# Optimization experiments

Measured on AMD Instinct MI355X. Metric: run time of the kernel, lower is better.

The kernel has to match this reference:

```python
import math
import jax, jax.numpy as jnp
import numpy as np

B, S, D, H = 4, 2048, 1024, 16
DK = D // H


def setup_inputs() -> dict:
    key = jax.random.key(0)
    ks = jax.random.split(key, 12)
    scale = 1.0 / math.sqrt(D)
    inp = {
        "query": jax.random.normal(ks[0], (B, S, D), jnp.float32),
        "key": jax.random.normal(ks[1], (B, S, D), jnp.float32),
        "value": jax.random.normal(ks[2], (B, S, D), jnp.float32),
        # causal mask, broadcasts over batch and (after unsqueeze) heads
        "mask": jnp.tril(jnp.ones((1, S, S), jnp.int32)),
        # torch Linear weights: [out_features, in_features]
        "Wq": jax.random.uniform(ks[3], (D, D), jnp.float32, -scale, scale),
        "bq": jax.random.uniform(ks[4], (D,), jnp.float32, -scale, scale),
        "Wk": jax.random.uniform(ks[5], (D, D), jnp.float32, -scale, scale),
        "bk": jax.random.uniform(ks[6], (D,), jnp.float32, -scale, scale),
        "Wv": jax.random.uniform(ks[7], (D, D), jnp.float32, -scale, scale),
        "bv": jax.random.uniform(ks[8], (D,), jnp.float32, -scale, scale),
        "Wo": jax.random.uniform(ks[9], (D, D), jnp.float32, -scale, scale),
        "bo": jax.random.uniform(ks[10], (D,), jnp.float32, -scale, scale),
    }
    return inp


def _proj(x, W, b):
    # torch Linear: x @ W.T + b, then split heads -> [B, H, S, DK]
    y = jnp.einsum('bsd,ed->bse', x, W) + b
    return y.reshape(x.shape[0], x.shape[1], H, DK).transpose(0, 2, 1, 3)


def reference(query, key, value, mask, Wq, bq, Wk, bk, Wv, bv, Wo, bo):
    q = _proj(query, Wq, bq)
    k = _proj(key, Wk, bk)
    v = _proj(value, Wv, bv)
    # scores: [B, H, S, S]
    scores = jnp.einsum('bhqd,bhkd->bhqk', q, k) / math.sqrt(DK)
    m = mask[:, None, :, :]  # mask.unsqueeze(1) -> broadcast over heads
    scores = jnp.where(m == 0, jnp.float32(-1e9), scores)
    prob = jax.nn.softmax(scores, axis=-1)
    # dropout is identity in eval mode
    x = jnp.einsum('bhqk,bhkd->bhqd', prob, v)
    x = x.transpose(0, 2, 1, 3).reshape(query.shape[0], -1, H * DK)
    return jnp.einsum('bsd,ed->bse', x, Wo) + bo
```

## Files before the change

kernel.cpp:

```cpp
#include <hip/hip_runtime.h>
#include <hip/hip_bf16.h>

#define DI __device__ __forceinline__

typedef __bf16 bf16x8 __attribute__((ext_vector_type(8)));
typedef unsigned short u16x8 __attribute__((ext_vector_type(8)));
typedef unsigned short u16x4 __attribute__((ext_vector_type(4)));
typedef unsigned int u32x4 __attribute__((ext_vector_type(4)));
typedef float f32x4 __attribute__((ext_vector_type(4)));
typedef float f32x16 __attribute__((ext_vector_type(16)));

constexpr int kB = 4, kS = 2048, kD = 1024, kH = 16;
constexpr int kM = kB * kS;

DI unsigned short f2bf(float f) {
  union { float f; unsigned u; } x; x.f = f;
  unsigned r = x.u + 0x7fffu + ((x.u >> 16) & 1u);
  return (unsigned short)(r >> 16);
}

DI f32x4 mfma16(u16x8 a, u16x8 b, f32x4 c) {
  return __builtin_amdgcn_mfma_f32_16x16x32_bf16(
      __builtin_bit_cast(bf16x8, a), __builtin_bit_cast(bf16x8, b), c, 0, 0, 0);
}
DI f32x16 mfma32(u16x8 a, u16x8 b, f32x16 c) {
  return __builtin_amdgcn_mfma_f32_32x32x16_bf16(
      __builtin_bit_cast(bf16x8, a), __builtin_bit_cast(bf16x8, b), c, 0, 0, 0);
}

DI void gload16(const unsigned short* g, unsigned short* l) {
  __builtin_amdgcn_global_load_lds(
      (__attribute__((address_space(1))) void*)g,
      (__attribute__((address_space(3))) void*)l, 16, 0, 0);
}

DI unsigned pkbf(float lo, float hi) {
  unsigned r;
  asm("v_cvt_pk_bf16_f32 %0, %1, %2" : "=v"(r) : "v"(lo), "v"(hi));
  return r;
}

__global__ __launch_bounds__(256) void conv_w(const float* __restrict__ s0,
                                              const float* __restrict__ s1,
                                              const float* __restrict__ s2,
                                              const float* __restrict__ s3,
                                              unsigned short* __restrict__ d) {
  const int j = blockIdx.y;
  const float* s = j == 0 ? s0 : j == 1 ? s1 : j == 2 ? s2 : s3;
  const size_t i = ((size_t)blockIdx.x * 256 + threadIdx.x) * 8;
  f32x4 a = *reinterpret_cast<const f32x4*>(s + i);
  f32x4 b = *reinterpret_cast<const f32x4*>(s + i + 4);
  u16x8 o;
#pragma unroll
  for (int jj = 0; jj < 4; ++jj) { o[jj] = f2bf(a[jj]); o[jj + 4] = f2bf(b[jj]); }
  *reinterpret_cast<u16x8*>(d + (size_t)j * 1048576 + i) = o;
}

__global__ __launch_bounds__(256) void proj_gemm(
    const float* __restrict__ A, const unsigned short* __restrict__ W,
    const float* __restrict__ bias, float scale, int vmode,
    unsigned short* __restrict__ O) {
  constexpr int K = kD, N = kD;
  __shared__ unsigned short As[128][64];
  __shared__ unsigned short Bs[2][128][64];

  const int lin = blockIdx.y * 8 + blockIdx.x;
  const int rm = (lin & 7) * 64 + (lin >> 3);
  const int n0 = (rm & 7) * 128, m0 = (rm >> 3) * 128;

  const int t = threadIdx.x;
  const int wave = t >> 6, lane = t & 63;
  const int wr = (wave >> 1) * 64, wc = (wave & 1) * 64;
  const int lrow = lane & 15, lkq = lane >> 4;

  const int rl = lane >> 3;
  const int bcs8 = ((lane & 7) ^ rl) * 8;
  const unsigned short* bsrc = W + ((size_t)(n0 + wave * 32 + rl)) * K + bcs8;
  unsigned short* bl = &Bs[0][0][0] + wave * 2048;

  const int ar_r = t >> 3, ar_c = t & 7;
  const int asw = (ar_c ^ (ar_r & 7)) * 8;
  const float* abase = A + (size_t)(m0 + ar_r) * K + ar_c * 8;

  f32x4 ar0[4], ar1[4];
#pragma unroll
  for (int i = 0; i < 4; ++i) {
    const float* ap = abase + (size_t)i * 32 * K;
    ar0[i] = *reinterpret_cast<const f32x4*>(ap);
    ar1[i] = *reinterpret_cast<const f32x4*>(ap + 4);
  }
#pragma unroll
  for (int i = 0; i < 4; ++i) gload16(bsrc + (size_t)i * 8 * K, bl + i * 512);

  f32x4 acc[4][4];
#pragma unroll
  for (int m = 0; m < 4; ++m)
#pragma unroll
    for (int n = 0; n < 4; ++n) acc[m][n] = f32x4{0.f, 0.f, 0.f, 0.f};

  for (int kt = 0; kt < K; kt += 64) {
    const int cb = (kt >> 6) & 1;
    __syncthreads();
#pragma unroll
    for (int i = 0; i < 4; ++i) {
      u32x4 w;
      w[0] = pkbf(ar0[i][0], ar0[i][1]);
      w[1] = pkbf(ar0[i][2], ar0[i][3]);
      w[2] = pkbf(ar1[i][0], ar1[i][1]);
      w[3] = pkbf(ar1[i][2], ar1[i][3]);
      *reinterpret_cast<u32x4*>(&As[ar_r + i * 32][asw]) = w;
    }
    __syncthreads();

    if (kt + 64 < K) {
#pragma unroll
      for (int i = 0; i < 4; ++i)
        gload16(bsrc + (size_t)i * 8 * K + kt + 64, bl + (cb ^ 1) * 8192 + i * 512);
#pragma unroll
      for (int i = 0; i < 4; ++i) {
        const float* ap = abase + (size_t)i * 32 * K + kt + 64;
        ar0[i] = *reinterpret_cast<const f32x4*>(ap);
        ar1[i] = *reinterpret_cast<const f32x4*>(ap + 4);
      }
    }

    u16x8 af[4][2], bf[4][2];
#pragma unroll
    for (int m = 0; m < 4; ++m) {
      const int row = wr + m * 16 + lrow;
#pragma unroll
      for (int kk = 0; kk < 2; ++kk)
        af[m][kk] = *reinterpret_cast<const u16x8*>(
            &As[row][((kk * 4 + lkq) ^ (row & 7)) * 8]);
    }
#pragma unroll
    for (int n = 0; n < 4; ++n) {
      const int row = wc + n * 16 + lrow;
#pragma unroll
      for (int kk = 0; kk < 2; ++kk)
        bf[n][kk] = *reinterpret_cast<const u16x8*>(
            &Bs[cb][row][((kk * 4 + lkq) ^ (row & 7)) * 8]);
    }
#pragma unroll
    for (int kk = 0; kk < 2; ++kk)
#pragma unroll
      for (int m = 0; m < 4; ++m)
#pragma unroll
        for (int n = 0; n < 4; ++n)
          acc[m][n] = mfma16(af[m][kk], bf[n][kk], acc[m][n]);
  }

#pragma unroll
  for (int n = 0; n < 4; ++n) {
    const int gc = n0 + wc + n * 16 + lrow;
    const float bvv = bias[gc];
#pragma unroll
    for (int m = 0; m < 4; ++m) {
      const int gr = m0 + wr + m * 16 + lkq * 4;
      if (vmode) {
        u16x4 o4;
#pragma unroll
        for (int j = 0; j < 4; ++j) o4[j] = f2bf(acc[m][n][j] + bvv);
        const size_t idx = ((size_t)(gr >> 11) * 1024 + gc) * 2048 + (gr & 2047);
        *reinterpret_cast<u16x4*>(O + idx) = o4;
      } else {
#pragma unroll
        for (int j = 0; j < 4; ++j)
          O[(size_t)(gr + j) * N + gc] = f2bf((acc[m][n][j] + bvv) * scale);
      }
    }
  }
}

__global__ __launch_bounds__(256) void gemm_o(const unsigned short* __restrict__ A,
                                              const unsigned short* __restrict__ W,
                                              const float* __restrict__ bias,
                                              float* __restrict__ C) {
  constexpr int K = kD, N = kD;
  __shared__ unsigned short As[2][128][64];
  __shared__ unsigned short Bs[2][128][64];

  const int lin = blockIdx.y * 8 + blockIdx.x;
  const int rm = (lin & 7) * 64 + (lin >> 3);
  const int n0 = (rm & 7) * 128, m0 = (rm >> 3) * 128;

  const int t = threadIdx.x;
  const int wave = t >> 6, lane = t & 63;
  const int wr = (wave >> 1) * 64, wc = (wave & 1) * 64;
  const int lrow = lane & 15, lkq = lane >> 4;

  const int rl = lane >> 3;
  const int cs8 = ((lane & 7) ^ rl) * 8;
  const unsigned short* asrc = A + ((size_t)(m0 + wave * 32 + rl)) * K + cs8;
  const unsigned short* bsrc = W + ((size_t)(n0 + wave * 32 + rl)) * K + cs8;
  unsigned short* al = &As[0][0][0] + wave * 2048;
  unsigned short* bl = &Bs[0][0][0] + wave * 2048;

#pragma unroll
  for (int i = 0; i < 4; ++i) {
    gload16(asrc + (size_t)i * 8 * K, al + i * 512);
    gload16(bsrc + (size_t)i * 8 * K, bl + i * 512);
  }

  f32x4 acc[4][4];
#pragma unroll
  for (int m = 0; m < 4; ++m)
#pragma unroll
    for (int n = 0; n < 4; ++n) acc[m][n] = f32x4{0.f, 0.f, 0.f, 0.f};

  for (int kt = 0; kt < K; kt += 64) {
    const int cb = (kt >> 6) & 1;
    __syncthreads();
    if (kt + 64 < K) {
#pragma unroll
      for (int i = 0; i < 4; ++i) {
        gload16(asrc + (size_t)i * 8 * K + kt + 64, al + (cb ^ 1) * 8192 + i * 512);
        gload16(bsrc + (size_t)i * 8 * K + kt + 64, bl + (cb ^ 1) * 8192 + i * 512);
      }
    }
    u16x8 af[4][2], bf[4][2];
#pragma unroll
    for (int m = 0; m < 4; ++m) {
      const int row = wr + m * 16 + lrow;
#pragma unroll
      for (int kk = 0; kk < 2; ++kk)
        af[m][kk] = *reinterpret_cast<const u16x8*>(
            &As[cb][row][((kk * 4 + lkq) ^ (row & 7)) * 8]);
    }
#pragma unroll
    for (int n = 0; n < 4; ++n) {
      const int row = wc + n * 16 + lrow;
#pragma unroll
      for (int kk = 0; kk < 2; ++kk)
        bf[n][kk] = *reinterpret_cast<const u16x8*>(
            &Bs[cb][row][((kk * 4 + lkq) ^ (row & 7)) * 8]);
    }
#pragma unroll
    for (int kk = 0; kk < 2; ++kk)
#pragma unroll
      for (int m = 0; m < 4; ++m)
#pragma unroll
        for (int n = 0; n < 4; ++n)
          acc[m][n] = mfma16(af[m][kk], bf[n][kk], acc[m][n]);
  }

#pragma unroll
  for (int n = 0; n < 4; ++n) {
    const int gc = n0 + wc + n * 16 + lrow;
    const float bvv = bias[gc];
#pragma unroll
    for (int m = 0; m < 4; ++m) {
      const int gr = m0 + wr + m * 16 + lkq * 4;
#pragma unroll
      for (int j = 0; j < 4; ++j)
        C[(size_t)(gr + j) * N + gc] = acc[m][n][j] + bvv;
    }
  }
}

__global__ __launch_bounds__(256) void attn_fused(
    const unsigned short* __restrict__ qb, const unsigned short* __restrict__ kb,
    const unsigned short* __restrict__ vbT, unsigned short* __restrict__ ob) {
  __shared__ unsigned short Ks[3][64][64];
  __shared__ unsigned short Vt[3][64][64];

  const int lin = blockIdx.y * 8 + blockIdx.x;
  const int rmap = (lin & 7) * 64 + (lin >> 3);
  const int bh = rmap >> 3;
  const int p = rmap & 7;
  const int b = bh >> 4, h = bh & 15;

  const int t = threadIdx.x;
  const int wave = t >> 6, lane = t & 63;
  const int lq = lane & 31, hi = lane >> 5;
  const int sw7 = lq & 7;

  const int np0 = 2 * (p + 1);
  constexpr int NT = 34;

  const int rl = lane >> 3;
  const int cs8 = ((lane & 7) ^ rl) * 8;
  const unsigned short* kbase =
      kb + ((size_t)(b * kS) + wave * 16 + rl) * kD + h * 64 + cs8;
  const unsigned short* vbase =
      vbT + ((size_t)(bh * 64) + wave * 16 + rl) * kS + cs8;

  int qt = p;
  int qw0 = qt * 128 + wave * 32;
  int qg = qw0 + lq;

  u16x8 bq[4];
  {
    const unsigned short* qrow = qb + ((size_t)(b * kS) + qg) * kD + h * 64;
#pragma unroll
    for (int s = 0; s < 4; ++s)
      bq[s] = *reinterpret_cast<const u16x8*>(qrow + s * 16 + hi * 8);
  }

  f32x16 oT0, oT1;
#pragma unroll
  for (int jj = 0; jj < 16; ++jj) { oT0[jj] = 0.f; oT1[jj] = 0.f; }
  float lsum = 0.f;

#define STAGE(ii)                                                      \
  {                                                                    \
    const int i_ = (ii);                                               \
    const int kv_ = (i_ < np0 ? i_ : i_ - np0) * 64;                   \
    unsigned short* kd_ = &Ks[i_ % 3][0][0] + wave * 1024;             \
    unsigned short* vd_ = &Vt[i_ % 3][0][0] + wave * 1024;             \
    const unsigned short* kp_ = kbase + (size_t)kv_ * kD;              \
    const unsigned short* vp_ = vbase + kv_;                           \
    gload16(kp_, kd_);                                                 \
    gload16(kp_ + (size_t)8 * kD, kd_ + 512);                          \
    gload16(vp_, vd_);                                                 \
    gload16(vp_ + (size_t)8 * kS, vd_ + 512);                          \
  }

  STAGE(0);
  STAGE(1);

  for (int i = 0; i < NT; ++i) {
    if (i == np0) {
      float ls = lsum + __shfl_xor(lsum, 32);
      const float rinv = 1.f / ls;
      unsigned short* orow = ob + ((size_t)(b * kS) + qg) * kD + h * 64 + 4 * hi;
#pragma unroll
      for (int d = 0; d < 2; ++d) {
        const f32x16& oo = d ? oT1 : oT0;
#pragma unroll
        for (int g = 0; g < 4; ++g) {
          u16x4 o4;
#pragma unroll
          for (int jj = 0; jj < 4; ++jj) o4[jj] = f2bf(oo[g * 4 + jj] * rinv);
          *reinterpret_cast<u16x4*>(orow + d * 32 + g * 8) = o4;
        }
      }
      qt = 15 - p;
      qw0 = qt * 128 + wave * 32;
      qg = qw0 + lq;
      const unsigned short* qrow = qb + ((size_t)(b * kS) + qg) * kD + h * 64;
#pragma unroll
      for (int s = 0; s < 4; ++s)
        bq[s] = *reinterpret_cast<const u16x8*>(qrow + s * 16 + hi * 8);
#pragma unroll
      for (int jj = 0; jj < 16; ++jj) { oT0[jj] = 0.f; oT1[jj] = 0.f; }
      lsum = 0.f;
    }

    if (i + 1 < NT) {
      asm volatile("s_waitcnt vmcnt(4)" ::: "memory");
    } else {
      asm volatile("s_waitcnt vmcnt(0)" ::: "memory");
    }
    __builtin_amdgcn_s_barrier();
    if (i + 2 < NT) STAGE(i + 2);

    const int k0 = (i < np0 ? i : i - np0) * 64;
    if (k0 <= qw0 + 31) {
      const unsigned short* Kc = &Ks[i % 3][0][0];
      const unsigned short* Vc = &Vt[i % 3][0][0];

      f32x16 st0, st1;
#pragma unroll
      for (int jj = 0; jj < 16; ++jj) { st0[jj] = 0.f; st1[jj] = 0.f; }
      __builtin_amdgcn_s_setprio(1);
#pragma unroll
      for (int s = 0; s < 4; ++s) {
        u16x8 ka = *reinterpret_cast<const u16x8*>(
            Kc + lq * 64 + (((2 * s + hi) ^ sw7) * 8));
        st0 = mfma32(ka, bq[s], st0);
      }
#pragma unroll
      for (int s = 0; s < 4; ++s) {
        u16x8 ka = *reinterpret_cast<const u16x8*>(
            Kc + (32 + lq) * 64 + (((2 * s + hi) ^ sw7) * 8));
        st1 = mfma32(ka, bq[s], st1);
      }
      __builtin_amdgcn_s_setprio(0);

      if (k0 + 63 <= qw0) {
#pragma unroll
        for (int r = 0; r < 16; ++r) {
          const float e0 = exp2f(st0[r]);
          const float e1 = exp2f(st1[r]);
          st0[r] = e0; st1[r] = e1;
          lsum += e0 + e1;
        }
      } else {
#pragma unroll
        for (int r = 0; r < 16; ++r) {
          const int kvl = (r & 3) + 8 * (r >> 2) + 4 * hi;
          const float e0 = (k0 + kvl > qg) ? 0.f : exp2f(st0[r]);
          const float e1 = (k0 + 32 + kvl > qg) ? 0.f : exp2f(st1[r]);
          st0[r] = e0; st1[r] = e1;
          lsum += e0 + e1;
        }
      }

      u16x8 pf[4];
#pragma unroll
      for (int s = 0; s < 4; ++s) {
        const f32x16& pc = (s < 2) ? st0 : st1;
        const int r0 = (s & 1) * 8;
        unsigned P0 = pkbf(pc[r0 + 0], pc[r0 + 1]);
        unsigned P1 = pkbf(pc[r0 + 2], pc[r0 + 3]);
        unsigned P2 = pkbf(pc[r0 + 4], pc[r0 + 5]);
        unsigned P3 = pkbf(pc[r0 + 6], pc[r0 + 7]);
        auto r02 = __builtin_amdgcn_permlane32_swap(P0, P2, false, false);
        auto r13 = __builtin_amdgcn_permlane32_swap(P1, P3, false, false);
        u32x4 w; w[0] = r02[0]; w[1] = r13[0]; w[2] = r02[1]; w[3] = r13[1];
        pf[s] = __builtin_bit_cast(u16x8, w);
      }

      __builtin_amdgcn_s_setprio(1);
#pragma unroll
      for (int s = 0; s < 4; ++s) {
        u16x8 va = *reinterpret_cast<const u16x8*>(
            Vc + lq * 64 + (((2 * s + hi) ^ sw7) * 8));
        oT0 = mfma32(va, pf[s], oT0);
      }
#pragma unroll
      for (int s = 0; s < 4; ++s) {
        u16x8 va = *reinterpret_cast<const u16x8*>(
            Vc + (32 + lq) * 64 + (((2 * s + hi) ^ sw7) * 8));
        oT1 = mfma32(va, pf[s], oT1);
      }
      __builtin_amdgcn_s_setprio(0);
    }
  }

  float ls = lsum + __shfl_xor(lsum, 32);
  const float rinv = 1.f / ls;
  unsigned short* orow = ob + ((size_t)(b * kS) + qg) * kD + h * 64 + 4 * hi;
#pragma unroll
  for (int d = 0; d < 2; ++d) {
    const f32x16& oo = d ? oT1 : oT0;
#pragma unroll
    for (int g = 0; g < 4; ++g) {
      u16x4 o4;
#pragma unroll
      for (int jj = 0; jj < 4; ++jj) o4[jj] = f2bf(oo[g * 4 + jj] * rinv);
      *reinterpret_cast<u16x4*>(orow + d * 32 + g * 8) = o4;
    }
  }
#undef STAGE
}

extern "C" void kernel_launch(void* const* d_in, const int* in_sizes, int n_in,
                              void* d_out, int out_size, void* d_ws, size_t ws_size,
                              hipStream_t stream) {
  (void)in_sizes; (void)n_in; (void)out_size; (void)ws_size;
  const float* query = (const float*)d_in[0];
  const float* key_ = (const float*)d_in[1];
  const float* value = (const float*)d_in[2];
  const float* Wq = (const float*)d_in[4];
  const float* bq = (const float*)d_in[5];
  const float* Wk = (const float*)d_in[6];
  const float* bk = (const float*)d_in[7];
  const float* Wv = (const float*)d_in[8];
  const float* bv = (const float*)d_in[9];
  const float* Wo = (const float*)d_in[10];
  const float* bo = (const float*)d_in[11];

  unsigned short* buf0 = (unsigned short*)d_ws;
  unsigned short* wcv = buf0 + (size_t)8 * 1024 * 1024;
  unsigned short* qbuf = wcv + (size_t)4 * 1024 * 1024;
  unsigned short* kbuf = qbuf + (size_t)8 * 1024 * 1024;
  unsigned short* vbT = kbuf + (size_t)8 * 1024 * 1024;

  constexpr float SCL2 = 0.18033688011112042f;

  dim3 gblk(8, 64);
  conv_w<<<dim3(512, 4), 256, 0, stream>>>(Wq, Wk, Wv, Wo, wcv);
  proj_gemm<<<gblk, 256, 0, stream>>>(query, wcv, bq, SCL2, 0, qbuf);
  proj_gemm<<<gblk, 256, 0, stream>>>(key_, wcv + 1048576, bk, 1.f, 0, kbuf);
  proj_gemm<<<gblk, 256, 0, stream>>>(value, wcv + 2 * 1048576, bv, 1.f, 1, vbT);
  attn_fused<<<gblk, 256, 0, stream>>>(qbuf, kbuf, vbT, buf0);
  gemm_o<<<gblk, 256, 0, stream>>>(buf0, wcv + 3 * 1048576, bo, (float*)d_out);
}
```

Before: 182.5 us.

## Enlarge attention KV tiles to 128 and use explicit waitcnt pipelining in GEMMs

The attention kernel moves from 64-row KV tiles in a 3-stage ring to 128-row tiles double-buffered, with a wider swizzled V layout. Each tile is now processed in 32-column chunks, and chunks fully past the causal diagonal are skipped. This halves the iteration count and the number of barriers. Both projection GEMMs replace __syncthreads with raw s_barrier plus explicit vmcnt/lgkmcnt waits, so the prefetch of the next stage can stay in flight across the barrier. The risks are shallower prefetch depth in attention and hand-counted waitcnt values that must match the number of outstanding loads.

After: 178.1 us. 1.02x faster.

```diff
diff --git a/kernel.cpp b/kernel.cpp
--- a/kernel.cpp
+++ b/kernel.cpp
@@ -100,7 +100,7 @@
 
   for (int kt = 0; kt < K; kt += 64) {
     const int cb = (kt >> 6) & 1;
-    __syncthreads();
+    __builtin_amdgcn_s_barrier();
 #pragma unroll
     for (int i = 0; i < 4; ++i) {
       u32x4 w;
@@ -110,7 +110,8 @@
       w[3] = pkbf(ar1[i][2], ar1[i][3]);
       *reinterpret_cast<u32x4*>(&As[ar_r + i * 32][asw]) = w;
     }
-    __syncthreads();
+    asm volatile("s_waitcnt lgkmcnt(0)" ::: "memory");
+    __builtin_amdgcn_s_barrier();
 
     if (kt + 64 < K) {
 #pragma unroll
@@ -122,6 +123,9 @@
         ar0[i] = *reinterpret_cast<const f32x4*>(ap);
         ar1[i] = *reinterpret_cast<const f32x4*>(ap + 4);
       }
+      asm volatile("s_waitcnt vmcnt(12)" ::: "memory");
+    } else {
+      asm volatile("s_waitcnt vmcnt(0)" ::: "memory");
     }
 
     u16x8 af[4][2], bf[4][2];
@@ -193,14 +197,20 @@
   const int cs8 = ((lane & 7) ^ rl) * 8;
   const unsigned short* asrc = A + ((size_t)(m0 + wave * 32 + rl)) * K + cs8;
   const unsigned short* bsrc = W + ((size_t)(n0 + wave * 32 + rl)) * K + cs8;
-  unsigned short* al = &As[0][0][0] + wave * 2048;
-  unsigned short* bl = &Bs[0][0][0] + wave * 2048;
-
-#pragma unroll
-  for (int i = 0; i < 4; ++i) {
-    gload16(asrc + (size_t)i * 8 * K, al + i * 512);
-    gload16(bsrc + (size_t)i * 8 * K, bl + i * 512);
-  }
+
+#define STAGEO(ii)                                                          \
+  {                                                                         \
+    const int i_ = (ii);                                                    \
+    const int kt_ = i_ * 64;                                                \
+    unsigned short* al_ = &As[i_ & 1][0][0] + wave * 2048;                  \
+    unsigned short* bl_ = &Bs[i_ & 1][0][0] + wave * 2048;                  \
+    _Pragma("unroll") for (int g_ = 0; g_ < 4; ++g_) {                      \
+      gload16(asrc + (size_t)g_ * 8 * K + kt_, al_ + g_ * 512);             \
+      gload16(bsrc + (size_t)g_ * 8 * K + kt_, bl_ + g_ * 512);             \
+    }                                                                       \
+  }
+
+  STAGEO(0);
 
   f32x4 acc[4][4];
 #pragma unroll
@@ -208,16 +218,15 @@
 #pragma unroll
     for (int n = 0; n < 4; ++n) acc[m][n] = f32x4{0.f, 0.f, 0.f, 0.f};
 
-  for (int kt = 0; kt < K; kt += 64) {
-    const int cb = (kt >> 6) & 1;
-    __syncthreads();
-    if (kt + 64 < K) {
-#pragma unroll
-      for (int i = 0; i < 4; ++i) {
-        gload16(asrc + (size_t)i * 8 * K + kt + 64, al + (cb ^ 1) * 8192 + i * 512);
-        gload16(bsrc + (size_t)i * 8 * K + kt + 64, bl + (cb ^ 1) * 8192 + i * 512);
-      }
-    }
+  for (int i = 0; i < 16; ++i) {
+    __builtin_amdgcn_s_barrier();
+    if (i + 1 < 16) {
+      STAGEO(i + 1);
+      asm volatile("s_waitcnt vmcnt(8)" ::: "memory");
+    } else {
+      asm volatile("s_waitcnt vmcnt(0)" ::: "memory");
+    }
+    const int cb = i & 1;
     u16x8 af[4][2], bf[4][2];
 #pragma unroll
     for (int m = 0; m < 4; ++m) {
@@ -243,6 +252,7 @@
         for (int n = 0; n < 4; ++n)
           acc[m][n] = mfma16(af[m][kk], bf[n][kk], acc[m][n]);
   }
+#undef STAGEO
 
 #pragma unroll
   for (int n = 0; n < 4; ++n) {
@@ -261,8 +271,8 @@
 __global__ __launch_bounds__(256) void attn_fused(
     const unsigned short* __restrict__ qb, const unsigned short* __restrict__ kb,
     const unsigned short* __restrict__ vbT, unsigned short* __restrict__ ob) {
-  __shared__ unsigned short Ks[3][64][64];
-  __shared__ unsigned short Vt[3][64][64];
+  __shared__ unsigned short Ks[2][128][64];
+  __shared__ unsigned short Vt[2][64][128];
 
   const int lin = blockIdx.y * 8 + blockIdx.x;
   const int rmap = (lin & 7) * 64 + (lin >> 3);
@@ -273,17 +283,38 @@
   const int t = threadIdx.x;
   const int wave = t >> 6, lane = t & 63;
   const int lq = lane & 31, hi = lane >> 5;
-  const int sw7 = lq & 7;
-
-  const int np0 = 2 * (p + 1);
-  constexpr int NT = 34;
-
-  const int rl = lane >> 3;
-  const int cs8 = ((lane & 7) ^ rl) * 8;
+  const int sw7 = lq & 7, sw15 = lq & 15;
+
+  const int np0 = p + 1;
+  constexpr int NT = 17;
+
+  const int krl = lane >> 3;
+  const int kcs = ((lane & 7) ^ krl) * 8;
   const unsigned short* kbase =
-      kb + ((size_t)(b * kS) + wave * 16 + rl) * kD + h * 64 + cs8;
-  const unsigned short* vbase =
-      vbT + ((size_t)(bh * 64) + wave * 16 + rl) * kS + cs8;
+      kb + ((size_t)(b * kS) + wave * 32 + krl) * kD + h * 64 + kcs;
+  const int vrl = lane >> 4, vc = lane & 15;
+  const size_t vrow = (size_t)(bh * 64) + wave * 16 + vrl;
+  const unsigned short* vsrc0 = vbT + (vrow + 0) * kS + (size_t)((vc ^ (vrl + 0)) * 8);
+  const unsigned short* vsrc1 = vbT + (vrow + 4) * kS + (size_t)((vc ^ (vrl + 4)) * 8);
+  const unsigned short* vsrc2 = vbT + (vrow + 8) * kS + (size_t)((vc ^ (vrl + 8)) * 8);
+  const unsigned short* vsrc3 = vbT + (vrow + 12) * kS + (size_t)((vc ^ (vrl + 12)) * 8);
+
+#define STAGE(ii)                                                  \
+  {                                                                \
+    const int i_ = (ii);                                           \
+    const int kv_ = (i_ < np0 ? i_ : i_ - np0) * 128;              \
+    unsigned short* kd_ = &Ks[i_ & 1][wave * 32][0];               \
+    const unsigned short* kp_ = kbase + (size_t)kv_ * kD;          \
+    gload16(kp_, kd_);                                             \
+    gload16(kp_ + (size_t)8 * kD, kd_ + 512);                      \
+    gload16(kp_ + (size_t)16 * kD, kd_ + 1024);                    \
+    gload16(kp_ + (size_t)24 * kD, kd_ + 1536);                    \
+    unsigned short* vd_ = &Vt[i_ & 1][wave * 16][0];               \
+    gload16(vsrc0 + kv_, vd_);                                     \
+    gload16(vsrc1 + kv_, vd_ + 512);                               \
+    gload16(vsrc2 + kv_, vd_ + 1024);                              \
+    gload16(vsrc3 + kv_, vd_ + 1536);                              \
+  }
 
   int qt = p;
   int qw0 = qt * 128 + wave * 32;
@@ -302,22 +333,7 @@
   for (int jj = 0; jj < 16; ++jj) { oT0[jj] = 0.f; oT1[jj] = 0.f; }
   float lsum = 0.f;
 
-#define STAGE(ii)                                                      \
-  {                                                                    \
-    const int i_ = (ii);                                               \
-    const int kv_ = (i_ < np0 ? i_ : i_ - np0) * 64;                   \
-    unsigned short* kd_ = &Ks[i_ % 3][0][0] + wave * 1024;             \
-    unsigned short* vd_ = &Vt[i_ % 3][0][0] + wave * 1024;             \
-    const unsigned short* kp_ = kbase + (size_t)kv_ * kD;              \
-    const unsigned short* vp_ = vbase + kv_;                           \
-    gload16(kp_, kd_);                                                 \
-    gload16(kp_ + (size_t)8 * kD, kd_ + 512);                          \
-    gload16(vp_, vd_);                                                 \
-    gload16(vp_ + (size_t)8 * kS, vd_ + 512);                          \
-  }
-
   STAGE(0);
-  STAGE(1);
 
   for (int i = 0; i < NT; ++i) {
     if (i == np0) {
@@ -347,87 +363,76 @@
       lsum = 0.f;
     }
 
+    __builtin_amdgcn_s_barrier();
     if (i + 1 < NT) {
-      asm volatile("s_waitcnt vmcnt(4)" ::: "memory");
+      STAGE(i + 1);
+      asm volatile("s_waitcnt vmcnt(8)" ::: "memory");
     } else {
       asm volatile("s_waitcnt vmcnt(0)" ::: "memory");
     }
-    __builtin_amdgcn_s_barrier();
-    if (i + 2 < NT) STAGE(i + 2);
-
-    const int k0 = (i < np0 ? i : i - np0) * 64;
+
+    const int k0 = (i < np0 ? i : i - np0) * 128;
     if (k0 <= qw0 + 31) {
-      const unsigned short* Kc = &Ks[i % 3][0][0];
-      const unsigned short* Vc = &Vt[i % 3][0][0];
-
-      f32x16 st0, st1;
-#pragma unroll
-      for (int jj = 0; jj < 16; ++jj) { st0[jj] = 0.f; st1[jj] = 0.f; }
-      __builtin_amdgcn_s_setprio(1);
-#pragma unroll
-      for (int s = 0; s < 4; ++s) {
-        u16x8 ka = *reinterpret_cast<const u16x8*>(
-            Kc + lq * 64 + (((2 * s + hi) ^ sw7) * 8));
-        st0 = mfma32(ka, bq[s], st0);
+      const unsigned short* Kc = &Ks[i & 1][0][0];
+      const unsigned short* Vc = &Vt[i & 1][0][0];
+
+#pragma unroll
+      for (int c = 0; c < 4; ++c) {
+        const int k0q = k0 + 32 * c;
+        if (k0q > qw0 + 31) continue;
+
+        f32x16 stq;
+#pragma unroll
+        for (int jj = 0; jj < 16; ++jj) stq[jj] = 0.f;
+        __builtin_amdgcn_s_setprio(1);
+#pragma unroll
+        for (int s = 0; s < 4; ++s) {
+          u16x8 ka = *reinterpret_cast<const u16x8*>(
+              Kc + (32 * c + lq) * 64 + (((2 * s + hi) ^ sw7) * 8));
+          stq = mfma32(ka, bq[s], stq);
+        }
+        __builtin_amdgcn_s_setprio(0);
+
+        if (k0q + 31 <= qw0) {
+#pragma unroll
+          for (int r = 0; r < 16; ++r) {
+            const float e = exp2f(stq[r]);
+            stq[r] = e;
+            lsum += e;
+          }
+        } else {
+#pragma unroll
+          for (int r = 0; r < 16; ++r) {
+            const int kvl = (r & 3) + 8 * (r >> 2) + 4 * hi;
+            const float e = (k0q + kvl > qg) ? 0.f : exp2f(stq[r]);
+            stq[r] = e;
+            lsum += e;
+          }
+        }
+
+        __builtin_amdgcn_s_setprio(1);
+#pragma unroll
+        for (int h2 = 0; h2 < 2; ++h2) {
+          const int r0 = h2 * 8;
+          unsigned P0 = pkbf(stq[r0 + 0], stq[r0 + 1]);
+          unsigned P1 = pkbf(stq[r0 + 2], stq[r0 + 3]);
+          unsigned P2 = pkbf(stq[r0 + 4], stq[r0 + 5]);
+          unsigned P3 = pkbf(stq[r0 + 6], stq[r0 + 7]);
+          auto r02 = __builtin_amdgcn_permlane32_swap(P0, P2, false, false);
+          auto r13 = __builtin_amdgcn_permlane32_swap(P1, P3, false, false);
+          u32x4 w; w[0] = r02[0]; w[1] = r13[0]; w[2] = r02[1]; w[3] = r13[1];
+          const u16x8 pf = __builtin_bit_cast(u16x8, w);
+          const int ch = ((2 * (2 * c + h2) + hi) ^ sw15) * 8;
+          u16x8 va0 = *reinterpret_cast<const u16x8*>(Vc + lq * 128 + ch);
+          u16x8 va1 = *reinterpret_cast<const u16x8*>(Vc + (32 + lq) * 128 + ch);
+          oT0 = mfma32(va0, pf, oT0);
+          oT1 = mfma32(va1, pf, oT1);
+        }
+        __builtin_amdgcn_s_setprio(0);
       }
-#pragma unroll
-      for (int s = 0; s < 4; ++s) {
-        u16x8 ka = *reinterpret_cast<const u16x8*>(
-            Kc + (32 + lq) * 64 + (((2 * s + hi) ^ sw7) * 8));
-        st1 = mfma32(ka, bq[s], st1);
-      }
-      __builtin_amdgcn_s_setprio(0);
-
-      if (k0 + 63 <= qw0) {
-#pragma unroll
-        for (int r = 0; r < 16; ++r) {
-          const float e0 = exp2f(st0[r]);
-          const float e1 = exp2f(st1[r]);
-          st0[r] = e0; st1[r] = e1;
-          lsum += e0 + e1;
-        }
-      } else {
-#pragma unroll
-        for (int r = 0; r < 16; ++r) {
-          const int kvl = (r & 3) + 8 * (r >> 2) + 4 * hi;
-          const float e0 = (k0 + kvl > qg) ? 0.f : exp2f(st0[r]);
-          const float e1 = (k0 + 32 + kvl > qg) ? 0.f : exp2f(st1[r]);
-          st0[r] = e0; st1[r] = e1;
-          lsum += e0 + e1;
-        }
-      }
-
-      u16x8 pf[4];
-#pragma unroll
-      for (int s = 0; s < 4; ++s) {
-        const f32x16& pc = (s < 2) ? st0 : st1;
-        const int r0 = (s & 1) * 8;
-        unsigned P0 = pkbf(pc[r0 + 0], pc[r0 + 1]);
-        unsigned P1 = pkbf(pc[r0 + 2], pc[r0 + 3]);
-        unsigned P2 = pkbf(pc[r0 + 4], pc[r0 + 5]);
-        unsigned P3 = pkbf(pc[r0 + 6], pc[r0 + 7]);
-        auto r02 = __builtin_amdgcn_permlane32_swap(P0, P2, false, false);
-        auto r13 = __builtin_amdgcn_permlane32_swap(P1, P3, false, false);
-        u32x4 w; w[0] = r02[0]; w[1] = r13[0]; w[2] = r02[1]; w[3] = r13[1];
-        pf[s] = __builtin_bit_cast(u16x8, w);
-      }
-
-      __builtin_amdgcn_s_setprio(1);
-#pragma unroll
-      for (int s = 0; s < 4; ++s) {
-        u16x8 va = *reinterpret_cast<const u16x8*>(
-            Vc + lq * 64 + (((2 * s + hi) ^ sw7) * 8));
-        oT0 = mfma32(va, pf[s], oT0);
-      }
-#pragma unroll
-      for (int s = 0; s < 4; ++s) {
-        u16x8 va = *reinterpret_cast<const u16x8*>(
-            Vc + (32 + lq) * 64 + (((2 * s + hi) ^ sw7) * 8));
-        oT1 = mfma32(va, pf[s], oT1);
-      }
-      __builtin_amdgcn_s_setprio(0);
-    }
-  }
+    }
+  }
+#undef STAGE
 
   float ls = lsum + __shfl_xor(lsum, 32);
   const float rinv = 1.f / ls;
@@ -443,7 +448,6 @@
       *reinterpret_cast<u16x4*>(orow + d * 32 + g * 8) = o4;
     }
   }
-#undef STAGE
 }
 
 extern "C" void kernel_launch(void* const* d_in, const int* in_sizes, int n_in,
```
